# Optimization experiments

Hardware: AMD Instinct MI355X
Metric: run time of the kernel (lower is better)

The kernel has to match this reference:

```python
import jax, jax.numpy as jnp
import numpy as np

B, S, H = 32, 2048, 1024

def setup_inputs() -> dict:
    key = jax.random.key(0)
    k0, k1, k2, k3 = jax.random.split(key, 4)
    hidden = jax.random.normal(k0, (B, H), dtype=jnp.float32)
    encoder_outputs = jax.random.normal(k1, (S, B, H), dtype=jnp.float32)
    # torch nn.Linear weight layout: [out_features, in_features]
    attn_W = jax.random.normal(k2, (H, 2 * H), dtype=jnp.float32) * (1.0 / np.sqrt(2 * H))
    attn_b = jnp.zeros((H,), dtype=jnp.float32)
    v_W = jax.random.normal(k3, (1, H), dtype=jnp.float32) * (1.0 / np.sqrt(H))
    return {"hidden": hidden, "encoder_outputs": encoder_outputs,
            "attn_W": attn_W, "attn_b": attn_b, "v_W": v_W}

def reference(hidden, encoder_outputs, attn_W, attn_b, v_W):
    # encoder_outputs: [S, B, H] -> [B, S, H]
    enc = jnp.transpose(encoder_outputs, (1, 0, 2))
    b, s, h = enc.shape
    # broadcast decoder hidden across seq dim (avoids explicit repeat copy)
    hid = jnp.broadcast_to(hidden[:, None, :], (b, s, h))
    cat = jnp.concatenate([hid, enc], axis=2)              # [B, S, 2H]
    energy = jnp.tanh(jnp.einsum('bsk,hk->bsh', cat, attn_W) + attn_b)  # [B, S, H]
    scores = jnp.einsum('bsh,oh->bso', energy, v_W)[..., 0]            # [B, S]
    attn_weights = jax.nn.softmax(scores, axis=1)                       # [B, S]
    context = jnp.einsum('bs,bsh->bh', attn_weights, enc)               # [B, H]
    return context, attn_weights
```

## Files before the change

### kernel.cpp

```cpp
#include <hip/hip_runtime.h>
#include <hip/hip_bf16.h>
#include <cstddef>

#define B_ 32
#define S_ 2048
#define H_ 1024

typedef short short8 __attribute__((ext_vector_type(8)));
typedef float floatx4 __attribute__((ext_vector_type(4)));

__device__ inline unsigned int cvt_pk_bf16(float a, float b) {
    unsigned int r;
    asm("v_cvt_pk_bf16_f32 %0, %1, %2" : "=v"(r) : "v"(a), "v"(b));
    return r;
}

__global__ void conv_enc(const float* __restrict__ enc, unsigned short* __restrict__ encb) {
    size_t i = (size_t)blockIdx.x * 256 + threadIdx.x;
    const float4* p = reinterpret_cast<const float4*>(enc) + i * 2;
    float4 v0 = p[0], v1 = p[1];
    union { short8 s; unsigned int u[4]; } o;
    o.u[0] = cvt_pk_bf16(v0.x, v0.y);
    o.u[1] = cvt_pk_bf16(v0.z, v0.w);
    o.u[2] = cvt_pk_bf16(v1.x, v1.y);
    o.u[3] = cvt_pk_bf16(v1.z, v1.w);
    reinterpret_cast<short8*>(encb)[i] = o.s;
}

__global__ void pack_w2(const float* __restrict__ W, unsigned short* __restrict__ W2) {
    int i = blockIdx.x * 256 + threadIdx.x;
    int n = i >> 8;
    int k4 = (i & 255) * 4;
    float4 v = *reinterpret_cast<const float4*>(W + (size_t)n * 2048 + 1024 + k4);
    uint2 o;
    o.x = cvt_pk_bf16(v.x, v.y);
    o.y = cvt_pk_bf16(v.z, v.w);
    *reinterpret_cast<uint2*>(W2 + (size_t)n * 1024 + k4) = o;
}

__global__ void hid_proj_kernel(const float* __restrict__ hidden,
                                const float* __restrict__ W,
                                const float* __restrict__ bias,
                                float* __restrict__ hp) {
    int h = blockIdx.x;
    int t = threadIdx.x;
    __shared__ float red[32][257];
    __shared__ float red2[32][8];
    float psum[32];
#pragma unroll
    for (int b = 0; b < 32; b++) psum[b] = 0.f;
    const float* wrow = W + (size_t)h * 2048;
    for (int c = 0; c < 4; c++) {
        int k = c * 256 + t;
        float w = wrow[k];
#pragma unroll
        for (int b = 0; b < 32; b++) psum[b] += hidden[b * 1024 + k] * w;
    }
#pragma unroll
    for (int b = 0; b < 32; b++) red[b][t] = psum[b];
    __syncthreads();
    {
        int b = t >> 3, j = t & 7;
        float s = 0.f;
#pragma unroll
        for (int q = 0; q < 32; q++) s += red[b][j * 32 + q];
        red2[b][j] = s;
    }
    __syncthreads();
    if (t < 32) {
        float tot = 0.f;
#pragma unroll
        for (int j = 0; j < 8; j++) tot += red2[t][j];
        hp[t * 1024 + h] = tot + bias[h];
    }
}

template<bool BF16A>
__global__ __launch_bounds__(256, 2) void score_gemm(
    const void* __restrict__ Ap,
    const unsigned short* __restrict__ W2,
    const float* __restrict__ hp,
    const float* __restrict__ vw,
    float* __restrict__ scores)
{
    __shared__ alignas(16) unsigned short As[128 * 64];
    __shared__ alignas(16) unsigned short Bs[256 * 64];
    __shared__ float scoreAcc[128][2];

    const int tid = threadIdx.x;
    const int lane = tid & 63;
    const int w = tid >> 6, wr = w >> 1, wc = w & 1;
    const int lr = lane & 15, lg = lane >> 4;
    const int mt = blockIdx.x;
    const int arow = tid >> 1, ahalf = tid & 1;
    const int lx = lr & 7;
    const int axk = arow & 7;
    const int bxk = tid & 7;

    const float* aF = (const float*)Ap + (size_t)(mt * 128 + arow) * H_ + ahalf * 32;
    const unsigned short* aB = (const unsigned short*)Ap + (size_t)(mt * 128 + arow) * H_ + ahalf * 32;

    if (tid < 128) { scoreAcc[tid][0] = 0.f; scoreAcc[tid][1] = 0.f; }

    short8 a8[4]; float4 af[8]; short8 b8[8];

    if (BF16A) {
        const short8* ap = reinterpret_cast<const short8*>(aB);
#pragma unroll
        for (int i = 0; i < 4; i++) a8[i] = ap[i];
    } else {
        const float4* ap = reinterpret_cast<const float4*>(aF);
#pragma unroll
        for (int i = 0; i < 8; i++) af[i] = ap[i];
    }
    {
        const short8* bp = reinterpret_cast<const short8*>(W2 + (size_t)tid * H_);
#pragma unroll
        for (int j = 0; j < 8; j++) b8[j] = bp[j];
    }

    for (int nt = 0; nt < 4; nt++) {
        floatx4 acc[4][8];
#pragma unroll
        for (int mi = 0; mi < 4; mi++)
#pragma unroll
            for (int ni = 0; ni < 8; ni++) acc[mi][ni] = (floatx4)0.f;

        for (int kt = 0; kt < 16; kt++) {
            __syncthreads();
            if (BF16A) {
#pragma unroll
                for (int i = 0; i < 4; i++)
                    *reinterpret_cast<short8*>(&As[arow * 64 + ((ahalf * 4 + i) ^ axk) * 8]) = a8[i];
            } else {
#pragma unroll
                for (int i = 0; i < 4; i++) {
                    union { short8 s; unsigned int u[4]; } o;
                    o.u[0] = cvt_pk_bf16(af[2 * i].x, af[2 * i].y);
                    o.u[1] = cvt_pk_bf16(af[2 * i].z, af[2 * i].w);
                    o.u[2] = cvt_pk_bf16(af[2 * i + 1].x, af[2 * i + 1].y);
                    o.u[3] = cvt_pk_bf16(af[2 * i + 1].z, af[2 * i + 1].w);
                    *reinterpret_cast<short8*>(&As[arow * 64 + ((ahalf * 4 + i) ^ axk) * 8]) = o.s;
                }
            }
#pragma unroll
            for (int j = 0; j < 8; j++)
                *reinterpret_cast<short8*>(&Bs[tid * 64 + ((j ^ bxk) * 8)]) = b8[j];
            __syncthreads();

            const int pnt = (kt < 15) ? nt : nt + 1;
            const int pkt = (kt < 15) ? kt + 1 : 0;
            if (pnt < 4) {
                if (BF16A) {
                    const short8* ap = reinterpret_cast<const short8*>(aB + pkt * 64);
#pragma unroll
                    for (int i = 0; i < 4; i++) a8[i] = ap[i];
                } else {
                    const float4* ap = reinterpret_cast<const float4*>(aF + pkt * 64);
#pragma unroll
                    for (int i = 0; i < 8; i++) af[i] = ap[i];
                }
                const short8* bp = reinterpret_cast<const short8*>(W2 + (size_t)(pnt * 256 + tid) * H_ + pkt * 64);
#pragma unroll
                for (int j = 0; j < 8; j++) b8[j] = bp[j];
            }

#pragma unroll
            for (int kk = 0; kk < 2; kk++) {
                const int g = (kk * 4 + lg) ^ lx;
                short8 afr[4], bfr[8];
#pragma unroll
                for (int mi = 0; mi < 4; mi++)
                    afr[mi] = *reinterpret_cast<const short8*>(&As[(wr * 64 + mi * 16 + lr) * 64 + g * 8]);
#pragma unroll
                for (int ni = 0; ni < 8; ni++)
                    bfr[ni] = *reinterpret_cast<const short8*>(&Bs[(wc * 128 + ni * 16 + lr) * 64 + g * 8]);
#pragma unroll
                for (int mi = 0; mi < 4; mi++)
#pragma unroll
                    for (int ni = 0; ni < 8; ni++)
                        acc[mi][ni] = __builtin_amdgcn_mfma_f32_16x16x32_bf16(
                            afr[mi], bfr[ni], acc[mi][ni], 0, 0, 0);
            }
        }

        const int colBase = nt * 256 + wc * 128;
        float vv[8];
#pragma unroll
        for (int ni = 0; ni < 8; ni++) vv[ni] = vw[colBase + ni * 16 + lr];
#pragma unroll
        for (int mi = 0; mi < 4; mi++) {
            const int row = wr * 64 + mi * 16 + lg * 4;
#pragma unroll
            for (int i = 0; i < 4; i++) {
                const int b = (row + i) & 31;
                const float* hprow = hp + b * H_ + colBase;
                float s = 0.f;
#pragma unroll
                for (int ni = 0; ni < 8; ni++) {
                    float e = acc[mi][ni][i] + hprow[ni * 16 + lr];
                    float e2 = __expf(2.0f * e);
                    float th = 1.0f - 2.0f * __builtin_amdgcn_rcpf(e2 + 1.0f);
                    s += th * vv[ni];
                }
                s += __shfl_xor(s, 1, 16);
                s += __shfl_xor(s, 2, 16);
                s += __shfl_xor(s, 4, 16);
                s += __shfl_xor(s, 8, 16);
                if (lr == 0) scoreAcc[row + i][wc] += s;
            }
        }
    }

    __syncthreads();
    if (tid < 128) {
        int m = mt * 128 + tid;
        scores[(m & 31) * S_ + (m >> 5)] = scoreAcc[tid][0] + scoreAcc[tid][1];
    }
}

__global__ void softmax_kernel(const float* __restrict__ scores, float* __restrict__ out) {
    int b = blockIdx.x, t = threadIdx.x;
    __shared__ float red[16];
    const float* row = scores + b * S_;
    float vals[8];
    float lmax = -1e30f;
#pragma unroll
    for (int i = 0; i < 8; i++) { vals[i] = row[i * 256 + t]; lmax = fmaxf(lmax, vals[i]); }
#pragma unroll
    for (int off = 32; off; off >>= 1) lmax = fmaxf(lmax, __shfl_xor(lmax, off, 64));
    if ((t & 63) == 0) red[t >> 6] = lmax;
    __syncthreads();
    float gmax = fmaxf(fmaxf(red[0], red[1]), fmaxf(red[2], red[3]));
    float lsum = 0.f;
#pragma unroll
    for (int i = 0; i < 8; i++) { vals[i] = __expf(vals[i] - gmax); lsum += vals[i]; }
#pragma unroll
    for (int off = 32; off; off >>= 1) lsum += __shfl_xor(lsum, off, 64);
    if ((t & 63) == 0) red[8 + (t >> 6)] = lsum;
    __syncthreads();
    float inv = 1.0f / (red[8] + red[9] + red[10] + red[11]);
#pragma unroll
    for (int i = 0; i < 8; i++) out[b * S_ + i * 256 + t] = vals[i] * inv;
}

__global__ void context_kernel(const float* __restrict__ enc,
                               const float* __restrict__ wts,
                               float* __restrict__ ctx) {
    int t = threadIdx.x;
    int hc = blockIdx.x & 3;
    int b = (blockIdx.x >> 2) & 31;
    int sc = blockIdx.x >> 7;
    int h = hc * 256 + t;
    const float* w = wts + b * S_ + sc * 128;
    const float* e = enc + (size_t)(sc * 128) * (B_ * H_) + b * H_ + h;
    float acc = 0.f;
#pragma unroll 4
    for (int s = 0; s < 128; s++)
        acc += w[s] * e[(size_t)s * (B_ * H_)];
    atomicAdd(&ctx[b * H_ + h], acc);
}

extern "C" void kernel_launch(void* const* d_in, const int* in_sizes, int n_in,
                              void* d_out, int out_size, void* d_ws, size_t ws_size,
                              hipStream_t stream) {
    const float* hidden = (const float*)d_in[0];
    const float* enc    = (const float*)d_in[1];
    const float* attn_W = (const float*)d_in[2];
    const float* attn_b = (const float*)d_in[3];
    const float* v_W    = (const float*)d_in[4];
    float* out = (float*)d_out;

    char* ws = (char*)d_ws;
    const size_t ENCB_BYTES = (size_t)S_ * B_ * H_ * 2;
    const size_t W2_BYTES   = (size_t)H_ * H_ * 2;
    const bool big = ws_size >= ENCB_BYTES + W2_BYTES + (1u << 20);

    unsigned short* encb = nullptr;
    unsigned short* W2bf;
    float* hp;
    float* scores;
    if (big) {
        encb   = (unsigned short*)ws;
        W2bf   = (unsigned short*)(ws + ENCB_BYTES);
        hp     = (float*)(ws + ENCB_BYTES + W2_BYTES);
        scores = (float*)(ws + ENCB_BYTES + W2_BYTES + (256u << 10));
    } else {
        W2bf   = (unsigned short*)ws;
        hp     = (float*)(ws + W2_BYTES);
        scores = (float*)(ws + W2_BYTES + (256u << 10));
    }

    pack_w2<<<1024, 256, 0, stream>>>(attn_W, W2bf);
    hid_proj_kernel<<<1024, 256, 0, stream>>>(hidden, attn_W, attn_b, hp);
    if (big) {
        conv_enc<<<32768, 256, 0, stream>>>(enc, encb);
        score_gemm<true><<<512, 256, 0, stream>>>((const void*)encb, W2bf, hp, v_W, scores);
    } else {
        score_gemm<false><<<512, 256, 0, stream>>>((const void*)enc, W2bf, hp, v_W, scores);
    }
    softmax_kernel<<<32, 256, 0, stream>>>(scores, out + B_ * H_);
    hipMemsetAsync(out, 0, B_ * H_ * sizeof(float), stream);
    context_kernel<<<2048, 256, 0, stream>>>(enc, out + B_ * H_, out);
}
```

Baseline: 706.1 us.

## Split score GEMM over N tiles with atomics; read bf16 encoder in context

The score GEMM goes from 512 blocks that each loop over four 256-wide N tiles to 4096 blocks of 128x128 tiles. Partial scores are combined with atomicAdd into a pre-zeroed buffer, and the launch bounds rise to 3 blocks per SM to improve occupancy and grid fill. The context kernel now reads the bf16 copy of the encoder when one is available, processes two h values per thread and uses half the blocks, which cuts its memory traffic. The costs are re-reading A across 8 N tiles, atomic contention on scores, and bf16 rounding in the context output.

```diff
diff --git a/kernel.cpp b/kernel.cpp
--- a/kernel.cpp
+++ b/kernel.cpp
@@ -76,7 +76,7 @@
 }
 
 template<bool BF16A>
-__global__ __launch_bounds__(256, 2) void score_gemm(
+__global__ __launch_bounds__(256, 3) void score_gemm(
     const void* __restrict__ Ap,
     const unsigned short* __restrict__ W2,
     const float* __restrict__ hp,
@@ -84,138 +84,127 @@
     float* __restrict__ scores)
 {
     __shared__ alignas(16) unsigned short As[128 * 64];
-    __shared__ alignas(16) unsigned short Bs[256 * 64];
-    __shared__ float scoreAcc[128][2];
+    __shared__ alignas(16) unsigned short Bs[128 * 64];
 
     const int tid = threadIdx.x;
     const int lane = tid & 63;
     const int w = tid >> 6, wr = w >> 1, wc = w & 1;
     const int lr = lane & 15, lg = lane >> 4;
-    const int mt = blockIdx.x;
-    const int arow = tid >> 1, ahalf = tid & 1;
+    const int bid = blockIdx.x;
+    const int nt = bid & 7, mt = bid >> 3;
+    const int row = tid >> 1, half = tid & 1;
+    const int xk = row & 7;
     const int lx = lr & 7;
-    const int axk = arow & 7;
-    const int bxk = tid & 7;
-
-    const float* aF = (const float*)Ap + (size_t)(mt * 128 + arow) * H_ + ahalf * 32;
-    const unsigned short* aB = (const unsigned short*)Ap + (size_t)(mt * 128 + arow) * H_ + ahalf * 32;
-
-    if (tid < 128) { scoreAcc[tid][0] = 0.f; scoreAcc[tid][1] = 0.f; }
-
-    short8 a8[4]; float4 af[8]; short8 b8[8];
+
+    const float* aF = (const float*)Ap + (size_t)(mt * 128 + row) * H_ + half * 32;
+    const unsigned short* aB = (const unsigned short*)Ap + (size_t)(mt * 128 + row) * H_ + half * 32;
+    const unsigned short* bP = W2 + (size_t)(nt * 128 + row) * H_ + half * 32;
+
+    short8 a8[4], b8[4]; float4 af[8];
 
     if (BF16A) {
-        const short8* ap = reinterpret_cast<const short8*>(aB);
-#pragma unroll
-        for (int i = 0; i < 4; i++) a8[i] = ap[i];
-    } else {
-        const float4* ap = reinterpret_cast<const float4*>(aF);
-#pragma unroll
-        for (int i = 0; i < 8; i++) af[i] = ap[i];
+        const short8* p = reinterpret_cast<const short8*>(aB);
+#pragma unroll
+        for (int i = 0; i < 4; i++) a8[i] = p[i];
+    } else {
+        const float4* p = reinterpret_cast<const float4*>(aF);
+#pragma unroll
+        for (int i = 0; i < 8; i++) af[i] = p[i];
     }
     {
-        const short8* bp = reinterpret_cast<const short8*>(W2 + (size_t)tid * H_);
-#pragma unroll
-        for (int j = 0; j < 8; j++) b8[j] = bp[j];
-    }
-
-    for (int nt = 0; nt < 4; nt++) {
-        floatx4 acc[4][8];
-#pragma unroll
-        for (int mi = 0; mi < 4; mi++)
-#pragma unroll
-            for (int ni = 0; ni < 8; ni++) acc[mi][ni] = (floatx4)0.f;
-
-        for (int kt = 0; kt < 16; kt++) {
-            __syncthreads();
+        const short8* p = reinterpret_cast<const short8*>(bP);
+#pragma unroll
+        for (int i = 0; i < 4; i++) b8[i] = p[i];
+    }
+
+    floatx4 acc[4][4];
+#pragma unroll
+    for (int mi = 0; mi < 4; mi++)
+#pragma unroll
+        for (int ni = 0; ni < 4; ni++) acc[mi][ni] = (floatx4)0.f;
+
+    for (int kt = 0; kt < 16; kt++) {
+        __syncthreads();
+        if (BF16A) {
+#pragma unroll
+            for (int i = 0; i < 4; i++)
+                *reinterpret_cast<short8*>(&As[row * 64 + ((half * 4 + i) ^ xk) * 8]) = a8[i];
+        } else {
+#pragma unroll
+            for (int i = 0; i < 4; i++) {
+                union { short8 s; unsigned int u[4]; } o;
+                o.u[0] = cvt_pk_bf16(af[2 * i].x, af[2 * i].y);
+                o.u[1] = cvt_pk_bf16(af[2 * i].z, af[2 * i].w);
+                o.u[2] = cvt_pk_bf16(af[2 * i + 1].x, af[2 * i + 1].y);
+                o.u[3] = cvt_pk_bf16(af[2 * i + 1].z, af[2 * i + 1].w);
+                *reinterpret_cast<short8*>(&As[row * 64 + ((half * 4 + i) ^ xk) * 8]) = o.s;
+            }
+        }
+#pragma unroll
+        for (int i = 0; i < 4; i++)
+            *reinterpret_cast<short8*>(&Bs[row * 64 + ((half * 4 + i) ^ xk) * 8]) = b8[i];
+        __syncthreads();
+
+        if (kt < 15) {
             if (BF16A) {
-#pragma unroll
-                for (int i = 0; i < 4; i++)
-                    *reinterpret_cast<short8*>(&As[arow * 64 + ((ahalf * 4 + i) ^ axk) * 8]) = a8[i];
+                const short8* p = reinterpret_cast<const short8*>(aB + (kt + 1) * 64);
+#pragma unroll
+                for (int i = 0; i < 4; i++) a8[i] = p[i];
             } else {
-#pragma unroll
-                for (int i = 0; i < 4; i++) {
-                    union { short8 s; unsigned int u[4]; } o;
-                    o.u[0] = cvt_pk_bf16(af[2 * i].x, af[2 * i].y);
-                    o.u[1] = cvt_pk_bf16(af[2 * i].z, af[2 * i].w);
-                    o.u[2] = cvt_pk_bf16(af[2 * i + 1].x, af[2 * i + 1].y);
-                    o.u[3] = cvt_pk_bf16(af[2 * i + 1].z, af[2 * i + 1].w);
-                    *reinterpret_cast<short8*>(&As[arow * 64 + ((ahalf * 4 + i) ^ axk) * 8]) = o.s;
-                }
+                const float4* p = reinterpret_cast<const float4*>(aF + (kt + 1) * 64);
+#pragma unroll
+                for (int i = 0; i < 8; i++) af[i] = p[i];
             }
-#pragma unroll
-            for (int j = 0; j < 8; j++)
-                *reinterpret_cast<short8*>(&Bs[tid * 64 + ((j ^ bxk) * 8)]) = b8[j];
-            __syncthreads();
-
-            const int pnt = (kt < 15) ? nt : nt + 1;
-            const int pkt = (kt < 15) ? kt + 1 : 0;
-            if (pnt < 4) {
-                if (BF16A) {
-                    const short8* ap = reinterpret_cast<const short8*>(aB + pkt * 64);
-#pragma unroll
-                    for (int i = 0; i < 4; i++) a8[i] = ap[i];
-                } else {
-                    const float4* ap = reinterpret_cast<const float4*>(aF + pkt * 64);
-#pragma unroll
-                    for (int i = 0; i < 8; i++) af[i] = ap[i];
-                }
-                const short8* bp = reinterpret_cast<const short8*>(W2 + (size_t)(pnt * 256 + tid) * H_ + pkt * 64);
-#pragma unroll
-                for (int j = 0; j < 8; j++) b8[j] = bp[j];
+            const short8* p = reinterpret_cast<const short8*>(bP + (kt + 1) * 64);
+#pragma unroll
+            for (int i = 0; i < 4; i++) b8[i] = p[i];
+        }
+
+#pragma unroll
+        for (int kk = 0; kk < 2; kk++) {
+            const int g = (kk * 4 + lg) ^ lx;
+            short8 afr[4], bfr[4];
+#pragma unroll
+            for (int mi = 0; mi < 4; mi++)
+                afr[mi] = *reinterpret_cast<const short8*>(&As[(wr * 64 + mi * 16 + lr) * 64 + g * 8]);
+#pragma unroll
+            for (int ni = 0; ni < 4; ni++)
+                bfr[ni] = *reinterpret_cast<const short8*>(&Bs[(wc * 64 + ni * 16 + lr) * 64 + g * 8]);
+#pragma unroll
+            for (int mi = 0; mi < 4; mi++)
+#pragma unroll
+                for (int ni = 0; ni < 4; ni++)
+                    acc[mi][ni] = __builtin_amdgcn_mfma_f32_16x16x32_bf16(
+                        afr[mi], bfr[ni], acc[mi][ni], 0, 0, 0);
+        }
+    }
+
+    const int colBase = nt * 128 + wc * 64;
+    float vv[4];
+#pragma unroll
+    for (int ni = 0; ni < 4; ni++) vv[ni] = vw[colBase + ni * 16 + lr];
+#pragma unroll
+    for (int mi = 0; mi < 4; mi++) {
+        const int rowm = wr * 64 + mi * 16 + lg * 4;
+#pragma unroll
+        for (int i = 0; i < 4; i++) {
+            const int m = mt * 128 + rowm + i;
+            const int b = m & 31, sidx = m >> 5;
+            const float* hprow = hp + b * H_ + colBase;
+            float s = 0.f;
+#pragma unroll
+            for (int ni = 0; ni < 4; ni++) {
+                float e = acc[mi][ni][i] + hprow[ni * 16 + lr];
+                float e2 = __expf(2.0f * e);
+                float th = 1.0f - 2.0f * __builtin_amdgcn_rcpf(e2 + 1.0f);
+                s += th * vv[ni];
             }
-
-#pragma unroll
-            for (int kk = 0; kk < 2; kk++) {
-                const int g = (kk * 4 + lg) ^ lx;
-                short8 afr[4], bfr[8];
-#pragma unroll
-                for (int mi = 0; mi < 4; mi++)
-                    afr[mi] = *reinterpret_cast<const short8*>(&As[(wr * 64 + mi * 16 + lr) * 64 + g * 8]);
-#pragma unroll
-                for (int ni = 0; ni < 8; ni++)
-                    bfr[ni] = *reinterpret_cast<const short8*>(&Bs[(wc * 128 + ni * 16 + lr) * 64 + g * 8]);
-#pragma unroll
-                for (int mi = 0; mi < 4; mi++)
-#pragma unroll
-                    for (int ni = 0; ni < 8; ni++)
-                        acc[mi][ni] = __builtin_amdgcn_mfma_f32_16x16x32_bf16(
-                            afr[mi], bfr[ni], acc[mi][ni], 0, 0, 0);
-            }
-        }
-
-        const int colBase = nt * 256 + wc * 128;
-        float vv[8];
-#pragma unroll
-        for (int ni = 0; ni < 8; ni++) vv[ni] = vw[colBase + ni * 16 + lr];
-#pragma unroll
-        for (int mi = 0; mi < 4; mi++) {
-            const int row = wr * 64 + mi * 16 + lg * 4;
-#pragma unroll
-            for (int i = 0; i < 4; i++) {
-                const int b = (row + i) & 31;
-                const float* hprow = hp + b * H_ + colBase;
-                float s = 0.f;
-#pragma unroll
-                for (int ni = 0; ni < 8; ni++) {
-                    float e = acc[mi][ni][i] + hprow[ni * 16 + lr];
-                    float e2 = __expf(2.0f * e);
-                    float th = 1.0f - 2.0f * __builtin_amdgcn_rcpf(e2 + 1.0f);
-                    s += th * vv[ni];
-                }
-                s += __shfl_xor(s, 1, 16);
-                s += __shfl_xor(s, 2, 16);
-                s += __shfl_xor(s, 4, 16);
-                s += __shfl_xor(s, 8, 16);
-                if (lr == 0) scoreAcc[row + i][wc] += s;
-            }
-        }
-    }
-
-    __syncthreads();
-    if (tid < 128) {
-        int m = mt * 128 + tid;
-        scores[(m & 31) * S_ + (m >> 5)] = scoreAcc[tid][0] + scoreAcc[tid][1];
+            s += __shfl_xor(s, 1, 16);
+            s += __shfl_xor(s, 2, 16);
+            s += __shfl_xor(s, 4, 16);
+            s += __shfl_xor(s, 8, 16);
+            if (lr == 0) atomicAdd(&scores[b * S_ + sidx], s);
+        }
     }
 }
 
@@ -244,21 +233,38 @@
     for (int i = 0; i < 8; i++) out[b * S_ + i * 256 + t] = vals[i] * inv;
 }
 
-__global__ void context_kernel(const float* __restrict__ enc,
+template<bool BF16E>
+__global__ void context_kernel(const void* __restrict__ encp,
                                const float* __restrict__ wts,
                                float* __restrict__ ctx) {
     int t = threadIdx.x;
-    int hc = blockIdx.x & 3;
-    int b = (blockIdx.x >> 2) & 31;
-    int sc = blockIdx.x >> 7;
-    int h = hc * 256 + t;
+    int hc = blockIdx.x & 1;
+    int b = (blockIdx.x >> 1) & 31;
+    int sc = blockIdx.x >> 6;
+    int h = hc * 512 + t * 2;
     const float* w = wts + b * S_ + sc * 128;
-    const float* e = enc + (size_t)(sc * 128) * (B_ * H_) + b * H_ + h;
-    float acc = 0.f;
-#pragma unroll 4
-    for (int s = 0; s < 128; s++)
-        acc += w[s] * e[(size_t)s * (B_ * H_)];
-    atomicAdd(&ctx[b * H_ + h], acc);
+    float acc0 = 0.f, acc1 = 0.f;
+    if (BF16E) {
+        const unsigned short* e = (const unsigned short*)encp
+            + (size_t)(sc * 128) * (B_ * H_) + b * H_ + h;
+#pragma unroll 8
+        for (int s = 0; s < 128; s++) {
+            unsigned int u = *reinterpret_cast<const unsigned int*>(e + (size_t)s * (B_ * H_));
+            float ws_ = w[s];
+            acc0 += ws_ * __uint_as_float(u << 16);
+            acc1 += ws_ * __uint_as_float(u & 0xffff0000u);
+        }
+    } else {
+        const float* e = (const float*)encp + (size_t)(sc * 128) * (B_ * H_) + b * H_ + h;
+#pragma unroll 8
+        for (int s = 0; s < 128; s++) {
+            float ws_ = w[s];
+            acc0 += ws_ * e[(size_t)s * (B_ * H_)];
+            acc1 += ws_ * e[(size_t)s * (B_ * H_) + 1];
+        }
+    }
+    atomicAdd(&ctx[b * H_ + h], acc0);
+    atomicAdd(&ctx[b * H_ + h + 1], acc1);
 }
 
 extern "C" void kernel_launch(void* const* d_in, const int* in_sizes, int n_in,
@@ -293,13 +299,18 @@
 
     pack_w2<<<1024, 256, 0, stream>>>(attn_W, W2bf);
     hid_proj_kernel<<<1024, 256, 0, stream>>>(hidden, attn_W, attn_b, hp);
+    hipMemsetAsync(scores, 0, B_ * S_ * sizeof(float), stream);
     if (big) {
         conv_enc<<<32768, 256, 0, stream>>>(enc, encb);
-        score_gemm<true><<<512, 256, 0, stream>>>((const void*)encb, W2bf, hp, v_W, scores);
-    } else {
-        score_gemm<false><<<512, 256, 0, stream>>>((const void*)enc, W2bf, hp, v_W, scores);
+        score_gemm<true><<<4096, 256, 0, stream>>>((const void*)encb, W2bf, hp, v_W, scores);
+    } else {
+        score_gemm<false><<<4096, 256, 0, stream>>>((const void*)enc, W2bf, hp, v_W, scores);
     }
     softmax_kernel<<<32, 256, 0, stream>>>(scores, out + B_ * H_);
     hipMemsetAsync(out, 0, B_ * H_ * sizeof(float), stream);
-    context_kernel<<<2048, 256, 0, stream>>>(enc, out + B_ * H_, out);
-}
+    if (big) {
+        context_kernel<true><<<1024, 256, 0, stream>>>((const void*)encb, out + B_ * H_, out);
+    } else {
+        context_kernel<false><<<1024, 256, 0, stream>>>((const void*)enc, out + B_ * H_, out);
+    }
+}
```

Result: no change. 699.3 us (-1.0%).
